# Kernel tuning notes

Hardware: AMD Instinct MI355X
Metric: run time of the kernel (lower is better)

## Reference

```python
import jax, jax.numpy as jnp
import numpy as np

B = 256       # decode batch
V = 50257     # per-model vocab size (GPT-2-class)
U = 65536     # union vocab size
M = 3         # number of ensembled models


def setup_inputs() -> dict:
    key = jax.random.key(0)
    ks = jax.random.split(key, 7)
    d = {}
    for i in range(M):
        d[f"logits{i}"] = jax.random.normal(ks[i], (B, V), dtype=jnp.float32)
    for i in range(M):
        # vocab_to_token_id mapping: model-local vocab index -> union vocab index
        d[f"map{i}"] = jax.random.randint(ks[M + i], (V,), 0, U, dtype=jnp.int32)
    d["weights"] = jnp.array([0.4, 0.35, 0.25], dtype=jnp.float32)
    return d


def reference(logits0, logits1, logits2, map0, map1, map2, weights):
    # union_probs[b, map_m[j]] += w_m * softmax(logits_m)[b, j]
    union = jnp.zeros((logits0.shape[0], U), dtype=logits0.dtype)
    for m, (lg, mp) in enumerate(zip((logits0, logits1, logits2),
                                     (map0, map1, map2))):
        p = jax.nn.softmax(lg, axis=-1)          # [B, V]
        union = union.at[:, mp].add(weights[m] * p)  # weighted scatter-add into [B, U]
    return union
```

## Files before the change

kernel.cpp:

```cpp
#include <hip/hip_runtime.h>

#define BB 256
#define VV 50257
#define UU 65536
#define MM 3
#define NT 1024

typedef float float4a __attribute__((ext_vector_type(4), aligned(4)));

#define WS_WINV   0
#define WS_HIST   3072
#define WS_OFF    7168
#define WS_CURSOR 11296
#define WS_SORTED 15392
#define WS_ET     618496
#define WS_NEED   77813248ull

__global__ __launch_bounds__(512) void row_sums_kernel(
    const float* __restrict__ l0, const float* __restrict__ l1,
    const float* __restrict__ l2, const float* __restrict__ weights,
    float* __restrict__ winv)
{
    const int bx = blockIdx.x;
    const int m  = bx >> 8;
    const int b  = bx & 255;
    const float* lg  = (m == 0) ? l0 : (m == 1) ? l1 : l2;
    const float* row = lg + (size_t)b * VV;
    const float4a* rowv = (const float4a*)row;

    const int nv4 = VV / 4;
    float partial = 0.0f;
    for (int i = threadIdx.x; i < nv4; i += 512) {
        float4a v = rowv[i];
        partial += __expf(v.x) + __expf(v.y) + __expf(v.z) + __expf(v.w);
    }
    if (threadIdx.x == 0) partial += __expf(row[VV - 1]);

    #pragma unroll
    for (int off = 32; off > 0; off >>= 1)
        partial += __shfl_down(partial, off, 64);

    __shared__ float smem[8];
    const int lane = threadIdx.x & 63;
    const int wv   = threadIdx.x >> 6;
    if (lane == 0) smem[wv] = partial;
    __syncthreads();
    if (threadIdx.x == 0) {
        float tot = 0.0f;
        #pragma unroll
        for (int w = 0; w < 8; ++w) tot += smem[w];
        winv[bx] = weights[m] / tot;
    }
}

__global__ __launch_bounds__(1024) void hist_count_kernel(
    const int* __restrict__ m0, const int* __restrict__ m1,
    const int* __restrict__ m2, int* __restrict__ hist)
{
    __shared__ int h[NT];
    for (int i = threadIdx.x; i < NT; i += 1024) h[i] = 0;
    __syncthreads();
    const int total = MM * VV;
    for (int idx = blockIdx.x * 1024 + threadIdx.x; idx < total;
         idx += gridDim.x * 1024) {
        const int m = idx / VV;
        const int j = idx - m * VV;
        const int* mp = (m == 0) ? m0 : (m == 1) ? m1 : m2;
        atomicAdd(&h[mp[j] >> 6], 1);
    }
    __syncthreads();
    for (int i = threadIdx.x; i < NT; i += 1024) atomicAdd(&hist[i], h[i]);
}

__global__ __launch_bounds__(1024) void prefix_kernel(
    const int* __restrict__ hist, int* __restrict__ off, int* __restrict__ cursor)
{
    __shared__ int s[NT];
    const int t = threadIdx.x;
    const int mine = hist[t];
    s[t] = mine;
    __syncthreads();
    for (int d = 1; d < NT; d <<= 1) {
        int v = (t >= d) ? s[t - d] : 0;
        __syncthreads();
        s[t] += v;
        __syncthreads();
    }
    const int excl = s[t] - mine;
    off[t] = excl;
    cursor[t] = excl;
    if (t == NT - 1) off[NT] = s[t];
}

__global__ __launch_bounds__(256) void sort_kernel(
    const int* __restrict__ m0, const int* __restrict__ m1,
    const int* __restrict__ m2, int* __restrict__ cursor,
    int* __restrict__ sorted)
{
    const int total = MM * VV;
    for (int idx = blockIdx.x * 256 + threadIdx.x; idx < total;
         idx += gridDim.x * 256) {
        const int m = idx / VV;
        const int j = idx - m * VV;
        const int* mp = (m == 0) ? m0 : (m == 1) ? m1 : m2;
        const int u = mp[j];
        const int pos = atomicAdd(&cursor[u >> 6], 1);
        sorted[pos] = (j << 8) | (m << 6) | (u & 63);
    }
}

__global__ __launch_bounds__(256) void transpose_exp_kernel(
    const float* __restrict__ l0, const float* __restrict__ l1,
    const float* __restrict__ l2, _Float16* __restrict__ ET)
{
    const int m  = blockIdx.z;
    const float* lg = (m == 0) ? l0 : (m == 1) ? l1 : l2;
    const int j0 = blockIdx.x * 64;
    const int b0 = blockIdx.y * 64;
    __shared__ float tile[64][65];
    const int lane = threadIdx.x & 63;
    const int sub  = threadIdx.x >> 6;

    const int j = j0 + lane;
    if (j < VV) {
        #pragma unroll
        for (int rr = 0; rr < 16; ++rr) {
            const int b = b0 + rr * 4 + sub;
            tile[lane][rr * 4 + sub] = __expf(lg[(size_t)b * VV + j]);
        }
    }
    __syncthreads();
    #pragma unroll
    for (int rr = 0; rr < 16; ++rr) {
        const int jj = rr * 4 + sub;
        const int jw = j0 + jj;
        if (jw < VV)
            ET[((size_t)m * VV + jw) * BB + b0 + lane] = (_Float16)tile[jj][lane];
    }
}

__global__ __launch_bounds__(256) void accumulate_kernel(
    const _Float16* __restrict__ ET, const int* __restrict__ sorted,
    const int* __restrict__ off, const float* __restrict__ winv,
    float* __restrict__ out)
{
    const int k = blockIdx.x;
    const int t = threadIdx.x;

    __shared__ float acc[64 * 256];
    for (int i = t; i < 64 * 256; i += 256) acc[i] = 0.0f;
    const float w0 = winv[0 * BB + t];
    const float w1 = winv[1 * BB + t];
    const float w2 = winv[2 * BB + t];
    __syncthreads();

    const int s = off[k], e = off[k + 1];
    #pragma unroll 4
    for (int i = s; i < e; ++i) {
        const int pack = sorted[i];
        const int ul = pack & 63;
        const int m  = (pack >> 6) & 3;
        const int j  = pack >> 8;
        const float ev = (float)ET[((size_t)m * VV + j) * BB + t];
        const float w  = (m == 0) ? w0 : (m == 1) ? w1 : w2;
        acc[ul * 256 + (t ^ (ul & 31))] += w * ev;
    }
    __syncthreads();

    const int u0 = k * 64;
    const int lane = t & 63, sub = t >> 6;
    #pragma unroll 4
    for (int c = 0; c < 64; ++c) {
        const int b = sub + c * 4;
        out[(size_t)b * UU + u0 + lane] = acc[lane * 256 + (b ^ (lane & 31))];
    }
}

#define FB_NBUCK 8
#define FB_BSZ   8192

__global__ __launch_bounds__(256) void fb_count_kernel(
    const int* __restrict__ m0, const int* __restrict__ m1,
    const int* __restrict__ m2, int* __restrict__ cnt)
{
    const int m = blockIdx.y;
    const int* mp = (m == 0) ? m0 : (m == 1) ? m1 : m2;
    __shared__ int hist[FB_NBUCK];
    if (threadIdx.x < FB_NBUCK) hist[threadIdx.x] = 0;
    __syncthreads();
    const int j = blockIdx.x * 256 + threadIdx.x;
    if (j < VV) atomicAdd(&hist[mp[j] >> 13], 1);
    __syncthreads();
    if (threadIdx.x < FB_NBUCK)
        atomicAdd(&cnt[m * FB_NBUCK + threadIdx.x], hist[threadIdx.x]);
}

__global__ void fb_prefix_kernel(const int* __restrict__ cnt,
                                 int* __restrict__ off, int* __restrict__ cursor)
{
    for (int m = 0; m < MM; ++m) {
        int acc = 0;
        for (int k = 0; k < FB_NBUCK; ++k) {
            off[m * (FB_NBUCK + 1) + k] = acc;
            cursor[m * FB_NBUCK + k]    = acc;
            acc += cnt[m * FB_NBUCK + k];
        }
        off[m * (FB_NBUCK + 1) + FB_NBUCK] = acc;
    }
}

__global__ __launch_bounds__(256) void fb_scatter_kernel(
    const int* __restrict__ m0, const int* __restrict__ m1,
    const int* __restrict__ m2, int* __restrict__ cursor,
    int* __restrict__ sorted)
{
    const int m = blockIdx.y;
    const int* mp = (m == 0) ? m0 : (m == 1) ? m1 : m2;
    int* srt = sorted + (size_t)m * VV;
    const int j = blockIdx.x * 256 + threadIdx.x;
    int u = 0, bucket = FB_NBUCK;
    if (j < VV) { u = mp[j]; bucket = u >> 13; }
    const int lane = threadIdx.x & 63;
    const unsigned long long lt = (1ull << lane) - 1ull;
    #pragma unroll
    for (int k = 0; k < FB_NBUCK; ++k) {
        unsigned long long mask = __ballot(bucket == k);
        if (mask) {
            int leader = __ffsll((long long)mask) - 1;
            int base = 0;
            if (lane == leader)
                base = atomicAdd(&cursor[m * FB_NBUCK + k], __popcll(mask));
            base = __shfl(base, leader, 64);
            if (bucket == k) {
                int pos = base + __popcll(mask & lt);
                srt[pos] = ((u & (FB_BSZ - 1)) << 16) | j;
            }
        }
    }
}

__global__ __launch_bounds__(512) void fb_accumulate_kernel(
    const float* __restrict__ l0, const float* __restrict__ l1,
    const float* __restrict__ l2,
    const int* __restrict__ sorted, const int* __restrict__ off,
    const float* __restrict__ winv, float* __restrict__ out)
{
    const int k = blockIdx.x;
    const int b = blockIdx.y;
    __shared__ float acc[FB_BSZ];
    for (int i = threadIdx.x; i < FB_BSZ; i += 512) acc[i] = 0.0f;
    __syncthreads();
    #pragma unroll
    for (int m = 0; m < MM; ++m) {
        const float* lg = (m == 0) ? l0 : (m == 1) ? l1 : l2;
        const float* row = lg + (size_t)b * VV;
        const int* srt = sorted + (size_t)m * VV;
        const float wv = winv[m * BB + b];
        const int s = off[m * (FB_NBUCK + 1) + k];
        const int e = off[m * (FB_NBUCK + 1) + k + 1];
        for (int i = s + threadIdx.x; i < e; i += 512) {
            const int pack = srt[i];
            atomicAdd(&acc[pack >> 16], wv * __expf(row[pack & 0xFFFF]));
        }
    }
    __syncthreads();
    float* orow = out + (size_t)b * UU + (size_t)k * FB_BSZ;
    for (int i = threadIdx.x; i < FB_BSZ; i += 512) orow[i] = acc[i];
}

extern "C" void kernel_launch(void* const* d_in, const int* in_sizes, int n_in,
                              void* d_out, int out_size, void* d_ws, size_t ws_size,
                              hipStream_t stream)
{
    const float* l0 = (const float*)d_in[0];
    const float* l1 = (const float*)d_in[1];
    const float* l2 = (const float*)d_in[2];
    const int*   m0 = (const int*)d_in[3];
    const int*   m1 = (const int*)d_in[4];
    const int*   m2 = (const int*)d_in[5];
    const float* w  = (const float*)d_in[6];
    float* out = (float*)d_out;
    char* ws = (char*)d_ws;

    if (ws_size >= WS_NEED) {
        float*    winv   = (float*)   (ws + WS_WINV);
        int*      hist   = (int*)     (ws + WS_HIST);
        int*      off    = (int*)     (ws + WS_OFF);
        int*      cursor = (int*)     (ws + WS_CURSOR);
        int*      sorted = (int*)     (ws + WS_SORTED);
        _Float16* ET     = (_Float16*)(ws + WS_ET);

        hipMemsetAsync(hist, 0, NT * sizeof(int), stream);

        row_sums_kernel<<<MM * BB, 512, 0, stream>>>(l0, l1, l2, w, winv);
        hist_count_kernel<<<64, 1024, 0, stream>>>(m0, m1, m2, hist);
        prefix_kernel<<<1, 1024, 0, stream>>>(hist, off, cursor);
        sort_kernel<<<256, 256, 0, stream>>>(m0, m1, m2, cursor, sorted);

        dim3 gtr((VV + 63) / 64, BB / 64, MM);
        transpose_exp_kernel<<<gtr, 256, 0, stream>>>(l0, l1, l2, ET);

        accumulate_kernel<<<NT, 256, 0, stream>>>(ET, sorted, off, winv, out);
    } else {
        float* winv   = (float*)(ws + 0);
        int*   cnt    = (int*)  (ws + 3072);
        int*   off    = (int*)  (ws + 3200);
        int*   cursor = (int*)  (ws + 3456);
        int*   sorted = (int*)  (ws + 3584);

        hipMemsetAsync(cnt, 0, MM * FB_NBUCK * sizeof(int), stream);
        row_sums_kernel<<<MM * BB, 512, 0, stream>>>(l0, l1, l2, w, winv);
        dim3 gmap((VV + 255) / 256, MM);
        fb_count_kernel<<<gmap, 256, 0, stream>>>(m0, m1, m2, cnt);
        fb_prefix_kernel<<<1, 1, 0, stream>>>(cnt, off, cursor);
        fb_scatter_kernel<<<gmap, 256, 0, stream>>>(m0, m1, m2, cursor, sorted);
        dim3 gacc(FB_NBUCK, BB);
        fb_accumulate_kernel<<<gacc, 512, 0, stream>>>(l0, l1, l2, sorted, off, winv, out);
    }
}
```

Measured before the change: 338.8 us.

## Fuse softmax row sums into transpose-exp and split accumulate across batch tiles

Drops the separate row-sum pass over the logits. The transpose-exp kernel now accumulates the per-row exponential sums into a global Z buffer with atomics, and the accumulate kernel derives weights/Z on the fly. The accumulate kernel is also re-gridded over 64-row batch tiles with a 16 KB shared accumulator, 16-way parallel over entries per block, with vectorised half4 loads and shared-memory atomics. This saves one full read of the logits and raises occupancy, at the cost of shared atomic contention, re-reading the sorted index list four times, and float-atomic nondeterminism in Z. Exponentials are not max-subtracted, as before.

```diff
diff --git a/kernel.cpp b/kernel.cpp
--- a/kernel.cpp
+++ b/kernel.cpp
@@ -7,8 +7,9 @@
 #define NT 1024
 
 typedef float float4a __attribute__((ext_vector_type(4), aligned(4)));
-
-#define WS_WINV   0
+typedef _Float16 half4 __attribute__((ext_vector_type(4)));
+
+#define WS_Z      0
 #define WS_HIST   3072
 #define WS_OFF    7168
 #define WS_CURSOR 11296
@@ -111,13 +112,15 @@
 
 __global__ __launch_bounds__(256) void transpose_exp_kernel(
     const float* __restrict__ l0, const float* __restrict__ l1,
-    const float* __restrict__ l2, _Float16* __restrict__ ET)
+    const float* __restrict__ l2, _Float16* __restrict__ ET,
+    float* __restrict__ Z)
 {
     const int m  = blockIdx.z;
     const float* lg = (m == 0) ? l0 : (m == 1) ? l1 : l2;
     const int j0 = blockIdx.x * 64;
     const int b0 = blockIdx.y * 64;
     __shared__ float tile[64][65];
+    __shared__ float ps[4][64];
     const int lane = threadIdx.x & 63;
     const int sub  = threadIdx.x >> 6;
 
@@ -130,49 +133,78 @@
         }
     }
     __syncthreads();
+    float partial = 0.0f;
     #pragma unroll
     for (int rr = 0; rr < 16; ++rr) {
         const int jj = rr * 4 + sub;
         const int jw = j0 + jj;
-        if (jw < VV)
-            ET[((size_t)m * VV + jw) * BB + b0 + lane] = (_Float16)tile[jj][lane];
-    }
-}
-
-__global__ __launch_bounds__(256) void accumulate_kernel(
+        if (jw < VV) {
+            const float v = tile[jj][lane];
+            ET[((size_t)m * VV + jw) * BB + b0 + lane] = (_Float16)v;
+            partial += v;
+        }
+    }
+    ps[sub][lane] = partial;
+    __syncthreads();
+    if (sub == 0)
+        atomicAdd(&Z[m * BB + b0 + lane],
+                  ps[0][lane] + ps[1][lane] + ps[2][lane] + ps[3][lane]);
+}
+
+__global__ __launch_bounds__(256, 8) void accumulate2_kernel(
     const _Float16* __restrict__ ET, const int* __restrict__ sorted,
-    const int* __restrict__ off, const float* __restrict__ winv,
-    float* __restrict__ out)
-{
-    const int k = blockIdx.x;
-    const int t = threadIdx.x;
-
-    __shared__ float acc[64 * 256];
-    for (int i = t; i < 64 * 256; i += 256) acc[i] = 0.0f;
-    const float w0 = winv[0 * BB + t];
-    const float w1 = winv[1 * BB + t];
-    const float w2 = winv[2 * BB + t];
-    __syncthreads();
-
-    const int s = off[k], e = off[k + 1];
-    #pragma unroll 4
-    for (int i = s; i < e; ++i) {
+    const int* __restrict__ off, const float* __restrict__ Z,
+    const float* __restrict__ weights, float* __restrict__ out)
+{
+    const int k  = blockIdx.x;
+    const int b0 = blockIdx.y * 64;
+    const int t  = threadIdx.x;
+
+    __shared__ float acc[64 * 64];
+    __shared__ float wl[3 * 64];
+
+    for (int i = t; i < 64 * 64; i += 256) acc[i] = 0.0f;
+    if (t < 192) {
+        const int mm = t >> 6, bl = t & 63;
+        wl[t] = weights[mm] / Z[mm * BB + b0 + bl];
+    }
+    __syncthreads();
+
+    const int g   = t & 15;
+    const int sub = t >> 4;
+    float4a wv0, wv1, wv2;
+    #pragma unroll
+    for (int c = 0; c < 4; ++c) {
+        wv0[c] = wl[0 * 64 + 4 * g + c];
+        wv1[c] = wl[1 * 64 + 4 * g + c];
+        wv2[c] = wl[2 * 64 + 4 * g + c];
+    }
+
+    const int s = off[k], eEnd = off[k + 1];
+    for (int i = s + sub; i < eEnd; i += 16) {
         const int pack = sorted[i];
         const int ul = pack & 63;
         const int m  = (pack >> 6) & 3;
         const int j  = pack >> 8;
-        const float ev = (float)ET[((size_t)m * VV + j) * BB + t];
-        const float w  = (m == 0) ? w0 : (m == 1) ? w1 : w2;
-        acc[ul * 256 + (t ^ (ul & 31))] += w * ev;
-    }
-    __syncthreads();
-
+        const half4 hv =
+            *(const half4*)(ET + ((size_t)m * VV + j) * BB + b0 + 4 * g);
+        const float4a wm = (m == 0) ? wv0 : (m == 1) ? wv1 : wv2;
+        const int rowbase = ul * 64;
+        #pragma unroll
+        for (int c = 0; c < 4; ++c) {
+            const int bl = 4 * g + c;
+            atomicAdd(&acc[rowbase + ((bl + ul) & 63)], wm[c] * (float)hv[c]);
+        }
+    }
+    __syncthreads();
+
+    const int lane = t & 63, s4 = t >> 6;
     const int u0 = k * 64;
-    const int lane = t & 63, sub = t >> 6;
     #pragma unroll 4
-    for (int c = 0; c < 64; ++c) {
-        const int b = sub + c * 4;
-        out[(size_t)b * UU + u0 + lane] = acc[lane * 256 + (b ^ (lane & 31))];
+    for (int r = 0; r < 16; ++r) {
+        const int bl = r * 4 + s4;
+        out[(size_t)(b0 + bl) * UU + u0 + lane] =
+            acc[lane * 64 + ((bl + lane) & 63)];
     }
 }
 
@@ -283,24 +315,24 @@
     char* ws = (char*)d_ws;
 
     if (ws_size >= WS_NEED) {
-        float*    winv   = (float*)   (ws + WS_WINV);
+        float*    Z      = (float*)   (ws + WS_Z);
         int*      hist   = (int*)     (ws + WS_HIST);
         int*      off    = (int*)     (ws + WS_OFF);
         int*      cursor = (int*)     (ws + WS_CURSOR);
         int*      sorted = (int*)     (ws + WS_SORTED);
         _Float16* ET     = (_Float16*)(ws + WS_ET);
 
-        hipMemsetAsync(hist, 0, NT * sizeof(int), stream);
-
-        row_sums_kernel<<<MM * BB, 512, 0, stream>>>(l0, l1, l2, w, winv);
+        hipMemsetAsync(ws, 0, 7168, stream);
+
         hist_count_kernel<<<64, 1024, 0, stream>>>(m0, m1, m2, hist);
         prefix_kernel<<<1, 1024, 0, stream>>>(hist, off, cursor);
         sort_kernel<<<256, 256, 0, stream>>>(m0, m1, m2, cursor, sorted);
 
         dim3 gtr((VV + 63) / 64, BB / 64, MM);
-        transpose_exp_kernel<<<gtr, 256, 0, stream>>>(l0, l1, l2, ET);
-
-        accumulate_kernel<<<NT, 256, 0, stream>>>(ET, sorted, off, winv, out);
+        transpose_exp_kernel<<<gtr, 256, 0, stream>>>(l0, l1, l2, ET, Z);
+
+        dim3 gacc(NT, BB / 64);
+        accumulate2_kernel<<<gacc, 256, 0, stream>>>(ET, sorted, off, Z, w, out);
     } else {
         float* winv   = (float*)(ws + 0);
         int*   cnt    = (int*)  (ws + 3072);
```

New measurement: 464.8 us. 37.2% more time.
